# Kernel tuning notes

Measured on AMD Instinct MI355X. Metric: run time of the kernel, lower is better.

The kernel has to match this reference:

```python
import jax, jax.numpy as jnp
import numpy as np
from functools import partial

B, IN, H, OUT, DEPTH = 4096, 1024, 2048, 1024, 8


def setup_inputs() -> dict:
    key = jax.random.key(0)
    ks = jax.random.split(key, 20)
    r = lambda k, shape: jax.random.normal(k, shape, dtype=jnp.float32)
    return {
        "x":  r(ks[0], (B, IN)),
        "W0": r(ks[1], (IN, H)) / np.sqrt(IN),  "b0": r(ks[2], (H,)) * 0.01,
        "W1": r(ks[3], (H, H)) / np.sqrt(H),    "b1": r(ks[4], (H,)) * 0.01,
        "cw1": r(ks[5], (DEPTH, H, H)), "cb1": r(ks[6], (H,)),
        "KW1": r(ks[7], (H, H)) / np.sqrt(H),  "Kb1": r(ks[8], (H,)) * 0.01,
        "W2": r(ks[9], (H, H)) / np.sqrt(H),   "b2": r(ks[10], (H,)) * 0.01,
        "cw2": r(ks[11], (DEPTH, H, H)), "cb2": r(ks[12], (H,)),
        "KW2": r(ks[13], (H, H)) / np.sqrt(H), "Kb2": r(ks[14], (H,)) * 0.01,
        "W3": r(ks[15], (H, OUT)) / np.sqrt(H), "b3": r(ks[16], (OUT,)) * 0.01,
    }


def _cosmic_processing(cw, batch, n_in, n_out):
    # state starts uniform over the n_in-dim 'cosmic' register, one per output j
    s0 = jnp.full((n_out, n_in), 1.0 / np.sqrt(n_in), dtype=cw.dtype)
    angles = cw[:, :, :3]  # (depth, n_out, 3): consciousness/intelligence/wisdom angles

    def step(s, ang):  # s: (n_out, n_in), ang: (n_out, 3)
        # circulant rotation: (M s)[i] = cos*s[i] - sin*s[i+1] + sin*s[i-1]
        for k in range(3):
            c = jnp.cos(ang[:, k])[:, None]
            si = jnp.sin(ang[:, k])[:, None]
            s = c * s - si * jnp.roll(s, -1, axis=1) + si * jnp.roll(s, 1, axis=1)
        return s, None

    s, _ = jax.lax.scan(step, s0, angles)
    prob = jnp.abs(s[:, 0]) ** 2  # (n_out,), sample-independent
    return jnp.broadcast_to(prob[None, :], (batch, n_out))


def _cosmic_layer(x, cw, cb, KW, Kb):
    classical = x @ KW + Kb
    cosmic = _cosmic_processing(cw, x.shape[0], x.shape[1], KW.shape[1])
    return jnp.tanh(classical + cosmic)


def reference(x, W0, b0, W1, b1, cw1, cb1, KW1, Kb1,
              W2, b2, cw2, cb2, KW2, Kb2, W3, b3):
    h = jax.nn.relu(x @ W0 + b0)
    h = jax.nn.relu(h @ W1 + b1)
    h = _cosmic_layer(h, cw1, cb1, KW1, Kb1)
    h = jax.nn.relu(h @ W2 + b2)
    h = _cosmic_layer(h, cw2, cb2, KW2, Kb2)
    return jax.nn.relu(h @ W3 + b3)
```

## Files before the change

### kernel.cpp

```cpp
#include <hip/hip_runtime.h>
#include <math.h>


typedef _Float16 f16;
typedef _Float16 f16x8 __attribute__((ext_vector_type(8)));
typedef _Float16 f16x4 __attribute__((ext_vector_type(4)));
typedef float f32x4 __attribute__((ext_vector_type(4)));

#define GLD16(gp, lp) __builtin_amdgcn_global_load_lds( \
    (const __attribute__((address_space(1))) unsigned int*)(gp), \
    (__attribute__((address_space(3))) unsigned int*)(lp), 16, 0, 0)

__device__ __forceinline__ float tanh_fast(float x) {
  return 1.0f - 2.0f / (__expf(2.0f * x) + 1.0f);
}

__global__ void cast_f32_f16(const float* __restrict__ in, f16* __restrict__ out, int n4) {
  int i = blockIdx.x * 256 + threadIdx.x;
  if (i < n4) {
    float4 v = ((const float4*)in)[i];
    f16x4 o = { (f16)v.x, (f16)v.y, (f16)v.z, (f16)v.w };
    ((f16x4*)out)[i] = o;
  }
}

struct TD { const float* src; f16* dst; int K; int N; };
struct TD6 { TD d[6]; };

__global__ void cast_transpose6(TD6 a) {
  TD d = a.d[blockIdx.z];
  const int bx = blockIdx.x * 64;
  const int by = blockIdx.y * 32;
  if (bx >= d.N || by >= d.K) return;
  __shared__ float tile[32][68];
  const int t = threadIdx.x;
#pragma unroll
  for (int pass = 0; pass < 2; ++pass) {
    int idx = t + pass * 256;
    int row = idx >> 4;
    int c4  = (idx & 15) * 4;
    float4 v = *(const float4*)&d.src[(size_t)(by + row) * d.N + bx + c4];
    *(float4*)&tile[row][c4] = v;
  }
  __syncthreads();
  const int nl = t >> 2;
  const int k8 = (t & 3) * 8;
  f16x8 o;
#pragma unroll
  for (int j = 0; j < 8; ++j) o[j] = (f16)tile[k8 + j][nl];
  *(f16x8*)&d.dst[(size_t)(bx + nl) * d.K + by + k8] = o;
}

__global__ void cosmic_pp(const float* __restrict__ cw, float* __restrict__ pp, int H) {
  int i = blockIdx.x * 256 + threadIdx.x;
  if (i >= 8 * H) return;
  const float* a = cw + (size_t)i * H;
  pp[i] = cosf(a[0]) * cosf(a[1]) * cosf(a[2]);
}
__global__ void cosmic_fin(const float* __restrict__ pp, float* __restrict__ prob, int H) {
  int r = blockIdx.x * 256 + threadIdx.x;
  if (r >= H) return;
  float p = 1.0f;
#pragma unroll
  for (int d = 0; d < 8; ++d) p *= pp[d * H + r];
  prob[r] = p * p / (float)H;
}

template <int EPI, int BM>
__global__ __launch_bounds__(256, 1)
void gemm_f16(const f16* __restrict__ A, const f16* __restrict__ BT,
              const float* __restrict__ bias, const float* __restrict__ prob,
              f16* __restrict__ Ch, float* __restrict__ Cf,
              int M, int N, int K, int GX) {
  constexpr int ASZ = BM * 64;
  constexpr int BSZ = 128 * 64;
  constexpr int MR  = BM / 32;
  constexpr int RA  = BM / 32;
  constexpr int NLD = RA + 4;
  __shared__ f16 lds[3 * (ASZ + BSZ)];
  f16* As = lds;
  f16* Bs = lds + 3 * ASZ;

  const int t = threadIdx.x;

  const int nwg = gridDim.x;
  const int bid = blockIdx.x;
  const int swz = (bid & 7) * (nwg >> 3) + (bid >> 3);
  const int bx = swz % GX;
  const int by = swz / GX;
  const int m0 = by * BM;
  const int n0 = bx * 128;

  auto stage_all = [&](int kt, int buf) {
    const int k0 = kt << 6;
#pragma unroll
    for (int q = 0; q < RA; ++q) {
      int F = q * 2048 + t * 8;
      int r = F >> 6, c = (F >> 3) & 7;
      GLD16(A + (size_t)(m0 + r) * K + k0 + ((c ^ (r & 7)) << 3), As + buf * ASZ + F);
    }
#pragma unroll
    for (int q = 0; q < 4; ++q) {
      int F = q * 2048 + t * 8;
      int r = F >> 6, c = (F >> 3) & 7;
      GLD16(BT + (size_t)(n0 + r) * K + k0 + ((c ^ (r & 7)) << 3), Bs + buf * BSZ + F);
    }
  };

  const int wave = t >> 6, lane = t & 63;
  const int wr = wave >> 1, wc = wave & 1;
  const int l16 = lane & 15, kq = lane >> 4;

  f32x4 acc[MR][4] = {};

  const int nt = K >> 6;
  stage_all(0, 0);
  stage_all(1, 1);
  int cur = 0;
  for (int kt = 0; kt < nt; ++kt) {
    if (kt + 1 < nt) {
      asm volatile("s_waitcnt vmcnt(%0)" :: "i"(NLD) : "memory");
    } else {
      asm volatile("s_waitcnt vmcnt(0)" ::: "memory");
    }
    __builtin_amdgcn_s_barrier();
    if (kt + 2 < nt) {
      int sb = cur + 2; if (sb >= 3) sb -= 3;
      stage_all(kt + 2, sb);
    }

    const f16* Ab = As + cur * ASZ;
    const f16* Bb = Bs + cur * BSZ;
    f16x8 a[2][MR], b[2][4];
#pragma unroll
    for (int s = 0; s < 2; ++s) {
      const int cc = s * 4 + kq;
#pragma unroll
      for (int mr = 0; mr < MR; ++mr) {
        int row = wr * (BM / 2) + mr * 16 + l16;
        a[s][mr] = *(const f16x8*)&Ab[row * 64 + ((cc ^ (row & 7)) << 3)];
      }
#pragma unroll
      for (int nr = 0; nr < 4; ++nr) {
        int row = wc * 64 + nr * 16 + l16;
        b[s][nr] = *(const f16x8*)&Bb[row * 64 + ((cc ^ (row & 7)) << 3)];
      }
      __builtin_amdgcn_sched_barrier(0);
    }
    asm volatile("s_waitcnt lgkmcnt(%0)" :: "i"(MR + 4) : "memory");
    __builtin_amdgcn_sched_barrier(0);
    __builtin_amdgcn_s_setprio(1);
#pragma unroll
    for (int mr = 0; mr < MR; ++mr)
#pragma unroll
      for (int nr = 0; nr < 4; ++nr)
        acc[mr][nr] = __builtin_amdgcn_mfma_f32_16x16x32_f16(a[0][mr], b[0][nr], acc[mr][nr], 0, 0, 0);
    __builtin_amdgcn_s_setprio(0);
    asm volatile("s_waitcnt lgkmcnt(0)" ::: "memory");
    __builtin_amdgcn_sched_barrier(0);
    __builtin_amdgcn_s_setprio(1);
#pragma unroll
    for (int mr = 0; mr < MR; ++mr)
#pragma unroll
      for (int nr = 0; nr < 4; ++nr)
        acc[mr][nr] = __builtin_amdgcn_mfma_f32_16x16x32_f16(a[1][mr], b[1][nr], acc[mr][nr], 0, 0, 0);
    __builtin_amdgcn_s_setprio(0);
    cur = (cur + 1 == 3) ? 0 : cur + 1;
  }

#pragma unroll
  for (int nr = 0; nr < 4; ++nr) {
    const int col = n0 + wc * 64 + nr * 16 + l16;
    float bn = bias[col];
    if (EPI == 1) bn += prob[col];
#pragma unroll
    for (int mr = 0; mr < MR; ++mr) {
      const int rbase = m0 + wr * (BM / 2) + mr * 16 + kq * 4;
#pragma unroll
      for (int q = 0; q < 4; ++q) {
        float v = acc[mr][nr][q] + bn;
        if (EPI == 1) v = tanh_fast(v);
        else v = fmaxf(v, 0.0f);
        if (EPI == 2) Cf[(size_t)(rbase + q) * N + col] = v;
        else Ch[(size_t)(rbase + q) * N + col] = (f16)v;
      }
    }
  }
}

extern "C" void kernel_launch(void* const* d_in, const int* in_sizes, int n_in,
                              void* d_out, int out_size, void* d_ws, size_t ws_size,
                              hipStream_t stream) {
  const float* x   = (const float*)d_in[0];
  const float* W0  = (const float*)d_in[1];
  const float* b0  = (const float*)d_in[2];
  const float* W1  = (const float*)d_in[3];
  const float* b1  = (const float*)d_in[4];
  const float* cw1 = (const float*)d_in[5];
  const float* KW1 = (const float*)d_in[7];
  const float* Kb1 = (const float*)d_in[8];
  const float* W2  = (const float*)d_in[9];
  const float* b2  = (const float*)d_in[10];
  const float* cw2 = (const float*)d_in[11];
  const float* KW2 = (const float*)d_in[13];
  const float* Kb2 = (const float*)d_in[14];
  const float* W3  = (const float*)d_in[15];
  const float* b3  = (const float*)d_in[16];

  const int B = 4096, IN = 1024, H = 2048, OUT = 1024;

  char* ws = (char*)d_ws;
  size_t off = 0;
  auto alloc = [&](size_t bytes) {
    char* p = ws + off;
    off = (off + bytes + 255) & ~(size_t)255;
    return p;
  };
  f16* xh    = (f16*)alloc((size_t)B * IN * 2);
  f16* W0T   = (f16*)alloc((size_t)H * IN * 2);
  f16* W1T   = (f16*)alloc((size_t)H * H * 2);
  f16* KW1T  = (f16*)alloc((size_t)H * H * 2);
  f16* W2T   = (f16*)alloc((size_t)H * H * 2);
  f16* KW2T  = (f16*)alloc((size_t)H * H * 2);
  f16* W3T   = (f16*)alloc((size_t)OUT * H * 2);
  f16* hA    = (f16*)alloc((size_t)B * H * 2);
  f16* hB    = (f16*)alloc((size_t)B * H * 2);
  float* p1  = (float*)alloc((size_t)H * 4);
  float* p2  = (float*)alloc((size_t)H * 4);
  float* pp  = (float*)alloc((size_t)8 * H * 4);
  (void)ws_size;

  cast_f32_f16<<<(B * IN / 4 + 255) / 256, 256, 0, stream>>>(x, xh, B * IN / 4);

  TD6 td;
  td.d[0] = { W0,  W0T,  IN, H };
  td.d[1] = { W1,  W1T,  H,  H };
  td.d[2] = { KW1, KW1T, H,  H };
  td.d[3] = { W2,  W2T,  H,  H };
  td.d[4] = { KW2, KW2T, H,  H };
  td.d[5] = { W3,  W3T,  H,  OUT };
  cast_transpose6<<<dim3(H / 64, H / 32, 6), 256, 0, stream>>>(td);

  cosmic_pp<<<(8 * H + 255) / 256, 256, 0, stream>>>(cw1, pp, H);
  cosmic_fin<<<(H + 255) / 256, 256, 0, stream>>>(pp, p1, H);
  cosmic_pp<<<(8 * H + 255) / 256, 256, 0, stream>>>(cw2, pp, H);
  cosmic_fin<<<(H + 255) / 256, 256, 0, stream>>>(pp, p2, H);

  {
    int gx = H / 128, gy = B / 256;
    dim3 g(gx * gy);
    gemm_f16<0, 256><<<g, 256, 0, stream>>>(xh, W0T, b0,  nullptr, hA, nullptr, B, H, IN, gx);
    gemm_f16<0, 256><<<g, 256, 0, stream>>>(hA, W1T, b1,  nullptr, hB, nullptr, B, H, H,  gx);
    gemm_f16<1, 256><<<g, 256, 0, stream>>>(hB, KW1T, Kb1, p1,     hA, nullptr, B, H, H,  gx);
    gemm_f16<0, 256><<<g, 256, 0, stream>>>(hA, W2T, b2,  nullptr, hB, nullptr, B, H, H,  gx);
    gemm_f16<1, 256><<<g, 256, 0, stream>>>(hB, KW2T, Kb2, p2,     hA, nullptr, B, H, H,  gx);
  }
  {
    int gx = OUT / 128, gy = B / 128;
    dim3 g(gx * gy);
    gemm_f16<2, 128><<<g, 256, 0, stream>>>(hA, W3T, b3, nullptr, nullptr, (float*)d_out, B, OUT, H, gx);
  }
}
```

Measured before the change: 242.1 us.

## Use 8-wave GEMM blocks with split-staged loads and register double-buffered LDS reads

Raises the GEMM workgroup from 4 to 8 waves, arranged 4x2, so each wave owns half as many M rows. The main loop now prefetches the second k-half LDS fragments while the first half's MFMAs issue. Global-to-LDS staging for tile kt+2 is split into two halves spread across the iteration, and launch bounds allow two blocks per CU. The goal is to hide LDS and global latency behind MFMA work and raise occupancy, at the cost of extra barriers per iteration and more complex wait-count bookkeeping.

```diff
diff --git a/kernel.cpp b/kernel.cpp
--- a/kernel.cpp
+++ b/kernel.cpp
@@ -67,16 +67,19 @@
 }
 
 template <int EPI, int BM>
-__global__ __launch_bounds__(256, 1)
+__global__ __launch_bounds__(512, 2)
 void gemm_f16(const f16* __restrict__ A, const f16* __restrict__ BT,
               const float* __restrict__ bias, const float* __restrict__ prob,
               f16* __restrict__ Ch, float* __restrict__ Cf,
               int M, int N, int K, int GX) {
-  constexpr int ASZ = BM * 64;
-  constexpr int BSZ = 128 * 64;
-  constexpr int MR  = BM / 32;
-  constexpr int RA  = BM / 32;
-  constexpr int NLD = RA + 4;
+  constexpr int ASZ  = BM * 64;
+  constexpr int BSZ  = 128 * 64;
+  constexpr int MR   = BM / 64;
+  constexpr int RA   = ASZ / 4096;
+  constexpr int RB   = BSZ / 4096;
+  constexpr int R    = RA + RB;
+  constexpr int HALF = R / 2;
+  constexpr int LG   = MR + 4;
   __shared__ f16 lds[3 * (ASZ + BSZ)];
   f16* As = lds;
   f16* Bs = lds + 3 * ASZ;
@@ -91,17 +94,14 @@
   const int m0 = by * BM;
   const int n0 = bx * 128;
 
-  auto stage_all = [&](int kt, int buf) {
+  auto stage_round = [&](int kt, int buf, int q) {
     const int k0 = kt << 6;
-#pragma unroll
-    for (int q = 0; q < RA; ++q) {
-      int F = q * 2048 + t * 8;
+    if (q < RA) {
+      int F = q * 4096 + t * 8;
       int r = F >> 6, c = (F >> 3) & 7;
       GLD16(A + (size_t)(m0 + r) * K + k0 + ((c ^ (r & 7)) << 3), As + buf * ASZ + F);
-    }
-#pragma unroll
-    for (int q = 0; q < 4; ++q) {
-      int F = q * 2048 + t * 8;
+    } else {
+      int F = (q - RA) * 4096 + t * 8;
       int r = F >> 6, c = (F >> 3) & 7;
       GLD16(BT + (size_t)(n0 + r) * K + k0 + ((c ^ (r & 7)) << 3), Bs + buf * BSZ + F);
     }
@@ -112,61 +112,76 @@
   const int l16 = lane & 15, kq = lane >> 4;
 
   f32x4 acc[MR][4] = {};
+  f16x8 a0[MR], b0[4], a1[MR], b1[4];
+
+  auto read_set = [&](int buf, int s, f16x8* ra, f16x8* rb) {
+#pragma unroll
+    for (int mr = 0; mr < MR; ++mr) {
+      int row = wr * (BM / 4) + mr * 16 + l16;
+      ra[mr] = *(const f16x8*)&As[buf * ASZ + row * 64 + (((s * 4 + kq) ^ (row & 7)) << 3)];
+    }
+#pragma unroll
+    for (int nr = 0; nr < 4; ++nr) {
+      int row = wc * 64 + nr * 16 + l16;
+      rb[nr] = *(const f16x8*)&Bs[buf * BSZ + row * 64 + (((s * 4 + kq) ^ (row & 7)) << 3)];
+    }
+  };
+  auto mfma_set = [&](const f16x8* ra, const f16x8* rb) {
+    __builtin_amdgcn_s_setprio(1);
+#pragma unroll
+    for (int mr = 0; mr < MR; ++mr)
+#pragma unroll
+      for (int nr = 0; nr < 4; ++nr)
+        acc[mr][nr] = __builtin_amdgcn_mfma_f32_16x16x32_f16(ra[mr], rb[nr], acc[mr][nr], 0, 0, 0);
+    __builtin_amdgcn_s_setprio(0);
+  };
 
   const int nt = K >> 6;
-  stage_all(0, 0);
-  stage_all(1, 1);
+#pragma unroll
+  for (int q = 0; q < R; ++q) stage_round(0, 0, q);
+#pragma unroll
+  for (int q = 0; q < R; ++q) stage_round(1, 1, q);
+  asm volatile("s_waitcnt vmcnt(%0)" :: "i"(R) : "memory");
+  __builtin_amdgcn_s_barrier();
+  read_set(0, 0, a0, b0);
+
   int cur = 0;
-  for (int kt = 0; kt < nt; ++kt) {
-    if (kt + 1 < nt) {
-      asm volatile("s_waitcnt vmcnt(%0)" :: "i"(NLD) : "memory");
+  for (int kt = 0; kt < nt - 1; ++kt) {
+    int nxt = cur + 1; if (nxt == 3) nxt = 0;
+    int sb  = cur + 2; if (sb  >= 3) sb -= 3;
+    const bool st = (kt + 2 < nt);
+    read_set(cur, 1, a1, b1);
+    if (st) {
+#pragma unroll
+      for (int q = 0; q < HALF; ++q) stage_round(kt + 2, sb, q);
+    }
+    __builtin_amdgcn_s_barrier();
+    asm volatile("s_waitcnt lgkmcnt(%0)" :: "i"(LG) : "memory");
+    __builtin_amdgcn_sched_barrier(0);
+    mfma_set(a0, b0);
+    __builtin_amdgcn_s_barrier();
+    if (st) {
+      asm volatile("s_waitcnt vmcnt(%0)" :: "i"(HALF) : "memory");
+#pragma unroll
+      for (int q = HALF; q < R; ++q) stage_round(kt + 2, sb, q);
     } else {
       asm volatile("s_waitcnt vmcnt(0)" ::: "memory");
     }
     __builtin_amdgcn_s_barrier();
-    if (kt + 2 < nt) {
-      int sb = cur + 2; if (sb >= 3) sb -= 3;
-      stage_all(kt + 2, sb);
-    }
-
-    const f16* Ab = As + cur * ASZ;
-    const f16* Bb = Bs + cur * BSZ;
-    f16x8 a[2][MR], b[2][4];
-#pragma unroll
-    for (int s = 0; s < 2; ++s) {
-      const int cc = s * 4 + kq;
-#pragma unroll
-      for (int mr = 0; mr < MR; ++mr) {
-        int row = wr * (BM / 2) + mr * 16 + l16;
-        a[s][mr] = *(const f16x8*)&Ab[row * 64 + ((cc ^ (row & 7)) << 3)];
-      }
-#pragma unroll
-      for (int nr = 0; nr < 4; ++nr) {
-        int row = wc * 64 + nr * 16 + l16;
-        b[s][nr] = *(const f16x8*)&Bb[row * 64 + ((cc ^ (row & 7)) << 3)];
-      }
-      __builtin_amdgcn_sched_barrier(0);
-    }
-    asm volatile("s_waitcnt lgkmcnt(%0)" :: "i"(MR + 4) : "memory");
+    read_set(nxt, 0, a0, b0);
+    asm volatile("s_waitcnt lgkmcnt(%0)" :: "i"(LG) : "memory");
     __builtin_amdgcn_sched_barrier(0);
-    __builtin_amdgcn_s_setprio(1);
-#pragma unroll
-    for (int mr = 0; mr < MR; ++mr)
-#pragma unroll
-      for (int nr = 0; nr < 4; ++nr)
-        acc[mr][nr] = __builtin_amdgcn_mfma_f32_16x16x32_f16(a[0][mr], b[0][nr], acc[mr][nr], 0, 0, 0);
-    __builtin_amdgcn_s_setprio(0);
-    asm volatile("s_waitcnt lgkmcnt(0)" ::: "memory");
-    __builtin_amdgcn_sched_barrier(0);
-    __builtin_amdgcn_s_setprio(1);
-#pragma unroll
-    for (int mr = 0; mr < MR; ++mr)
-#pragma unroll
-      for (int nr = 0; nr < 4; ++nr)
-        acc[mr][nr] = __builtin_amdgcn_mfma_f32_16x16x32_f16(a[1][mr], b[1][nr], acc[mr][nr], 0, 0, 0);
-    __builtin_amdgcn_s_setprio(0);
-    cur = (cur + 1 == 3) ? 0 : cur + 1;
-  }
+    mfma_set(a1, b1);
+    __builtin_amdgcn_s_barrier();
+    cur = nxt;
+  }
+  read_set(cur, 1, a1, b1);
+  asm volatile("s_waitcnt lgkmcnt(%0)" :: "i"(LG) : "memory");
+  __builtin_amdgcn_sched_barrier(0);
+  mfma_set(a0, b0);
+  asm volatile("s_waitcnt lgkmcnt(0)" ::: "memory");
+  __builtin_amdgcn_sched_barrier(0);
+  mfma_set(a1, b1);
 
 #pragma unroll
   for (int nr = 0; nr < 4; ++nr) {
@@ -175,7 +190,7 @@
     if (EPI == 1) bn += prob[col];
 #pragma unroll
     for (int mr = 0; mr < MR; ++mr) {
-      const int rbase = m0 + wr * (BM / 2) + mr * 16 + kq * 4;
+      const int rbase = m0 + wr * (BM / 4) + mr * 16 + kq * 4;
 #pragma unroll
       for (int q = 0; q < 4; ++q) {
         float v = acc[mr][nr][q] + bn;
@@ -249,15 +264,15 @@
   {
     int gx = H / 128, gy = B / 256;
     dim3 g(gx * gy);
-    gemm_f16<0, 256><<<g, 256, 0, stream>>>(xh, W0T, b0,  nullptr, hA, nullptr, B, H, IN, gx);
-    gemm_f16<0, 256><<<g, 256, 0, stream>>>(hA, W1T, b1,  nullptr, hB, nullptr, B, H, H,  gx);
-    gemm_f16<1, 256><<<g, 256, 0, stream>>>(hB, KW1T, Kb1, p1,     hA, nullptr, B, H, H,  gx);
-    gemm_f16<0, 256><<<g, 256, 0, stream>>>(hA, W2T, b2,  nullptr, hB, nullptr, B, H, H,  gx);
-    gemm_f16<1, 256><<<g, 256, 0, stream>>>(hB, KW2T, Kb2, p2,     hA, nullptr, B, H, H,  gx);
+    gemm_f16<0, 256><<<g, 512, 0, stream>>>(xh, W0T, b0,  nullptr, hA, nullptr, B, H, IN, gx);
+    gemm_f16<0, 256><<<g, 512, 0, stream>>>(hA, W1T, b1,  nullptr, hB, nullptr, B, H, H,  gx);
+    gemm_f16<1, 256><<<g, 512, 0, stream>>>(hB, KW1T, Kb1, p1,     hA, nullptr, B, H, H,  gx);
+    gemm_f16<0, 256><<<g, 512, 0, stream>>>(hA, W2T, b2,  nullptr, hB, nullptr, B, H, H,  gx);
+    gemm_f16<1, 256><<<g, 512, 0, stream>>>(hB, KW2T, Kb2, p2,     hA, nullptr, B, H, H,  gx);
   }
   {
     int gx = OUT / 128, gy = B / 128;
     dim3 g(gx * gy);
-    gemm_f16<2, 128><<<g, 256, 0, stream>>>(hA, W3T, b3, nullptr, nullptr, (float*)d_out, B, OUT, H, gx);
-  }
-}
+    gemm_f16<2, 128><<<g, 512, 0, stream>>>(hA, W3T, b3, nullptr, nullptr, (float*)d_out, B, OUT, H, gx);
+  }
+}
```

After: 227.7 us. 1.06x faster.

## Use 512-thread GEMM blocks with BK=32 tiles and merge cosmic kernels

Applied to the files above, without the earlier changes.

Reworks the GEMM template to use 8 waves per block (512 threads) with configurable block and warp tiling, and halves the K-tile to 32 so LDS per buffer shrinks. This allows several blocks per CU for more latency hiding. The cost is twice as many barriers per K and one LDS read batch per tile instead of two overlapped sub-steps. Separately, the two cosmic probability computations are fused into single launches.

```diff
diff --git a/kernel.cpp b/kernel.cpp
--- a/kernel.cpp
+++ b/kernel.cpp
@@ -51,32 +51,41 @@
   *(f16x8*)&d.dst[(size_t)(bx + nl) * d.K + by + k8] = o;
 }
 
-__global__ void cosmic_pp(const float* __restrict__ cw, float* __restrict__ pp, int H) {
+__global__ void cosmic_pp2(const float* __restrict__ cw1, const float* __restrict__ cw2,
+                           float* __restrict__ pp, int H) {
   int i = blockIdx.x * 256 + threadIdx.x;
-  if (i >= 8 * H) return;
-  const float* a = cw + (size_t)i * H;
+  if (i >= 16 * H) return;
+  const float* cw = (i < 8 * H) ? cw1 : cw2;
+  int j = (i < 8 * H) ? i : i - 8 * H;
+  const float* a = cw + (size_t)j * H;
   pp[i] = cosf(a[0]) * cosf(a[1]) * cosf(a[2]);
 }
-__global__ void cosmic_fin(const float* __restrict__ pp, float* __restrict__ prob, int H) {
+__global__ void cosmic_fin2(const float* __restrict__ pp, float* __restrict__ p1,
+                            float* __restrict__ p2, int H) {
   int r = blockIdx.x * 256 + threadIdx.x;
-  if (r >= H) return;
+  if (r >= 2 * H) return;
+  int rr = (r < H) ? r : r - H;
+  const float* base = pp + ((r < H) ? 0 : 8 * H);
   float p = 1.0f;
 #pragma unroll
-  for (int d = 0; d < 8; ++d) p *= pp[d * H + r];
-  prob[r] = p * p / (float)H;
-}
-
-template <int EPI, int BM>
-__global__ __launch_bounds__(256, 1)
+  for (int d = 0; d < 8; ++d) p *= base[d * H + rr];
+  float v = p * p / (float)H;
+  if (r < H) p1[rr] = v; else p2[rr] = v;
+}
+
+template <int EPI, int BM, int BN, int WM, int WN, int MINW>
+__global__ __launch_bounds__(512, MINW)
 void gemm_f16(const f16* __restrict__ A, const f16* __restrict__ BT,
               const float* __restrict__ bias, const float* __restrict__ prob,
               f16* __restrict__ Ch, float* __restrict__ Cf,
               int M, int N, int K, int GX) {
-  constexpr int ASZ = BM * 64;
-  constexpr int BSZ = 128 * 64;
-  constexpr int MR  = BM / 32;
-  constexpr int RA  = BM / 32;
-  constexpr int NLD = RA + 4;
+  constexpr int ASZ = BM * 32;
+  constexpr int BSZ = BN * 32;
+  constexpr int MR  = BM / WM / 16;
+  constexpr int NR  = BN / WN / 16;
+  constexpr int RA  = ASZ / 4096;
+  constexpr int RB  = BSZ / 4096;
+  constexpr int NLD = RA + RB;
   __shared__ f16 lds[3 * (ASZ + BSZ)];
   f16* As = lds;
   f16* Bs = lds + 3 * ASZ;
@@ -89,31 +98,31 @@
   const int bx = swz % GX;
   const int by = swz / GX;
   const int m0 = by * BM;
-  const int n0 = bx * 128;
+  const int n0 = bx * BN;
 
   auto stage_all = [&](int kt, int buf) {
-    const int k0 = kt << 6;
+    const int k0 = kt << 5;
 #pragma unroll
     for (int q = 0; q < RA; ++q) {
-      int F = q * 2048 + t * 8;
-      int r = F >> 6, c = (F >> 3) & 7;
-      GLD16(A + (size_t)(m0 + r) * K + k0 + ((c ^ (r & 7)) << 3), As + buf * ASZ + F);
-    }
-#pragma unroll
-    for (int q = 0; q < 4; ++q) {
-      int F = q * 2048 + t * 8;
-      int r = F >> 6, c = (F >> 3) & 7;
-      GLD16(BT + (size_t)(n0 + r) * K + k0 + ((c ^ (r & 7)) << 3), Bs + buf * BSZ + F);
+      int F = q * 4096 + t * 8;
+      int r = F >> 5, c = (F >> 3) & 3;
+      GLD16(A + (size_t)(m0 + r) * K + k0 + ((c ^ (r & 3)) << 3), As + buf * ASZ + F);
+    }
+#pragma unroll
+    for (int q = 0; q < RB; ++q) {
+      int F = q * 4096 + t * 8;
+      int r = F >> 5, c = (F >> 3) & 3;
+      GLD16(BT + (size_t)(n0 + r) * K + k0 + ((c ^ (r & 3)) << 3), Bs + buf * BSZ + F);
     }
   };
 
   const int wave = t >> 6, lane = t & 63;
-  const int wr = wave >> 1, wc = wave & 1;
+  const int wr = wave / WN, wc = wave % WN;
   const int l16 = lane & 15, kq = lane >> 4;
 
-  f32x4 acc[MR][4] = {};
-
-  const int nt = K >> 6;
+  f32x4 acc[MR][NR] = {};
+
+  const int nt = K >> 5;
   stage_all(0, 0);
   stage_all(1, 1);
   int cur = 0;
@@ -131,51 +140,37 @@
 
     const f16* Ab = As + cur * ASZ;
     const f16* Bb = Bs + cur * BSZ;
-    f16x8 a[2][MR], b[2][4];
-#pragma unroll
-    for (int s = 0; s < 2; ++s) {
-      const int cc = s * 4 + kq;
-#pragma unroll
-      for (int mr = 0; mr < MR; ++mr) {
-        int row = wr * (BM / 2) + mr * 16 + l16;
-        a[s][mr] = *(const f16x8*)&Ab[row * 64 + ((cc ^ (row & 7)) << 3)];
-      }
-#pragma unroll
-      for (int nr = 0; nr < 4; ++nr) {
-        int row = wc * 64 + nr * 16 + l16;
-        b[s][nr] = *(const f16x8*)&Bb[row * 64 + ((cc ^ (row & 7)) << 3)];
-      }
-      __builtin_amdgcn_sched_barrier(0);
-    }
-    asm volatile("s_waitcnt lgkmcnt(%0)" :: "i"(MR + 4) : "memory");
-    __builtin_amdgcn_sched_barrier(0);
-    __builtin_amdgcn_s_setprio(1);
-#pragma unroll
-    for (int mr = 0; mr < MR; ++mr)
-#pragma unroll
-      for (int nr = 0; nr < 4; ++nr)
-        acc[mr][nr] = __builtin_amdgcn_mfma_f32_16x16x32_f16(a[0][mr], b[0][nr], acc[mr][nr], 0, 0, 0);
-    __builtin_amdgcn_s_setprio(0);
+    f16x8 a[MR], b[NR];
+#pragma unroll
+    for (int mr = 0; mr < MR; ++mr) {
+      int row = wr * (MR * 16) + mr * 16 + l16;
+      a[mr] = *(const f16x8*)&Ab[row * 32 + ((kq ^ (row & 3)) << 3)];
+    }
+#pragma unroll
+    for (int nr = 0; nr < NR; ++nr) {
+      int row = wc * (NR * 16) + nr * 16 + l16;
+      b[nr] = *(const f16x8*)&Bb[row * 32 + ((kq ^ (row & 3)) << 3)];
+    }
     asm volatile("s_waitcnt lgkmcnt(0)" ::: "memory");
     __builtin_amdgcn_sched_barrier(0);
     __builtin_amdgcn_s_setprio(1);
 #pragma unroll
     for (int mr = 0; mr < MR; ++mr)
 #pragma unroll
-      for (int nr = 0; nr < 4; ++nr)
-        acc[mr][nr] = __builtin_amdgcn_mfma_f32_16x16x32_f16(a[1][mr], b[1][nr], acc[mr][nr], 0, 0, 0);
+      for (int nr = 0; nr < NR; ++nr)
+        acc[mr][nr] = __builtin_amdgcn_mfma_f32_16x16x32_f16(a[mr], b[nr], acc[mr][nr], 0, 0, 0);
     __builtin_amdgcn_s_setprio(0);
     cur = (cur + 1 == 3) ? 0 : cur + 1;
   }
 
 #pragma unroll
-  for (int nr = 0; nr < 4; ++nr) {
-    const int col = n0 + wc * 64 + nr * 16 + l16;
+  for (int nr = 0; nr < NR; ++nr) {
+    const int col = n0 + wc * (NR * 16) + nr * 16 + l16;
     float bn = bias[col];
     if (EPI == 1) bn += prob[col];
 #pragma unroll
     for (int mr = 0; mr < MR; ++mr) {
-      const int rbase = m0 + wr * (BM / 2) + mr * 16 + kq * 4;
+      const int rbase = m0 + wr * (MR * 16) + mr * 16 + kq * 4;
 #pragma unroll
       for (int q = 0; q < 4; ++q) {
         float v = acc[mr][nr][q] + bn;
@@ -227,7 +222,7 @@
   f16* hB    = (f16*)alloc((size_t)B * H * 2);
   float* p1  = (float*)alloc((size_t)H * 4);
   float* p2  = (float*)alloc((size_t)H * 4);
-  float* pp  = (float*)alloc((size_t)8 * H * 4);
+  float* pp  = (float*)alloc((size_t)16 * H * 4);
   (void)ws_size;
 
   cast_f32_f16<<<(B * IN / 4 + 255) / 256, 256, 0, stream>>>(x, xh, B * IN / 4);
@@ -241,23 +236,21 @@
   td.d[5] = { W3,  W3T,  H,  OUT };
   cast_transpose6<<<dim3(H / 64, H / 32, 6), 256, 0, stream>>>(td);
 
-  cosmic_pp<<<(8 * H + 255) / 256, 256, 0, stream>>>(cw1, pp, H);
-  cosmic_fin<<<(H + 255) / 256, 256, 0, stream>>>(pp, p1, H);
-  cosmic_pp<<<(8 * H + 255) / 256, 256, 0, stream>>>(cw2, pp, H);
-  cosmic_fin<<<(H + 255) / 256, 256, 0, stream>>>(pp, p2, H);
+  cosmic_pp2<<<(16 * H + 255) / 256, 256, 0, stream>>>(cw1, cw2, pp, H);
+  cosmic_fin2<<<(2 * H + 255) / 256, 256, 0, stream>>>(pp, p1, p2, H);
 
   {
     int gx = H / 128, gy = B / 256;
     dim3 g(gx * gy);
-    gemm_f16<0, 256><<<g, 256, 0, stream>>>(xh, W0T, b0,  nullptr, hA, nullptr, B, H, IN, gx);
-    gemm_f16<0, 256><<<g, 256, 0, stream>>>(hA, W1T, b1,  nullptr, hB, nullptr, B, H, H,  gx);
-    gemm_f16<1, 256><<<g, 256, 0, stream>>>(hB, KW1T, Kb1, p1,     hA, nullptr, B, H, H,  gx);
-    gemm_f16<0, 256><<<g, 256, 0, stream>>>(hA, W2T, b2,  nullptr, hB, nullptr, B, H, H,  gx);
-    gemm_f16<1, 256><<<g, 256, 0, stream>>>(hB, KW2T, Kb2, p2,     hA, nullptr, B, H, H,  gx);
+    gemm_f16<0, 256, 128, 4, 2, 4><<<g, 512, 0, stream>>>(xh, W0T, b0,  nullptr, hA, nullptr, B, H, IN, gx);
+    gemm_f16<0, 256, 128, 4, 2, 4><<<g, 512, 0, stream>>>(hA, W1T, b1,  nullptr, hB, nullptr, B, H, H,  gx);
+    gemm_f16<1, 256, 128, 4, 2, 4><<<g, 512, 0, stream>>>(hB, KW1T, Kb1, p1,     hA, nullptr, B, H, H,  gx);
+    gemm_f16<0, 256, 128, 4, 2, 4><<<g, 512, 0, stream>>>(hA, W2T, b2,  nullptr, hB, nullptr, B, H, H,  gx);
+    gemm_f16<1, 256, 128, 4, 2, 4><<<g, 512, 0, stream>>>(hB, KW2T, Kb2, p2,     hA, nullptr, B, H, H,  gx);
   }
   {
     int gx = OUT / 128, gy = B / 128;
     dim3 g(gx * gy);
-    gemm_f16<2, 128><<<g, 256, 0, stream>>>(hA, W3T, b3, nullptr, nullptr, (float*)d_out, B, OUT, H, gx);
-  }
-}
+    gemm_f16<2, 128, 128, 2, 4, 2><<<g, 512, 0, stream>>>(hA, W3T, b3, nullptr, nullptr, (float*)d_out, B, OUT, H, gx);
+  }
+}
```

Result: slower. 249.6 us (+3.1%).
